# Kernel optimization log

Measured on AMD Instinct MI355X. Metric: run time of the kernel, lower is better.

## Reference

```python
import jax, jax.numpy as jnp
import numpy as np

D = 4  # max horizontal displacement


def setup_inputs() -> dict:
    key = jax.random.key(0)
    k1, k2 = jax.random.split(key)
    feat1 = jax.random.normal(k1, (8, 256, 96, 320), dtype=jnp.float32)
    feat2 = jax.random.normal(k2, (8, 256, 96, 320), dtype=jnp.float32)
    return {"feat1": feat1, "feat2": feat2}


def reference(feat1, feat2):
    B, C, H, W = feat1.shape
    # zero-pad feat2 along width by D on each side
    feat2_padded = jnp.pad(feat2, ((0, 0), (0, 0), (0, 0), (D, D)))
    costs = []
    for i in range(2 * D + 1):  # small fixed loop over 2d+1 shifts
        feat2_slice = jax.lax.dynamic_slice_in_dim(feat2_padded, i, W, axis=3)
        # channel-mean correlation -> (B, H, W)
        costs.append(jnp.mean(feat1 * feat2_slice, axis=1))
    # stack shifts as channels -> (B, 2d+1, H, W)
    return jnp.stack(costs, axis=1)
```

## Files before the change

### kernel.cpp

```cpp
#include <hip/hip_runtime.h>


constexpr int B  = 8;
constexpr int C  = 256;
constexpr int H  = 96;
constexpr int W  = 320;
constexpr int NS = 9;
constexpr int QT = W / 4;
constexpr int RPB = 3;
constexpr int NTH = RPB * QT;
constexpr int HW  = H * W;
constexpr int PADW = W + 8;
constexpr int NSTEP = C / 2;

__global__ __launch_bounds__(NTH, 1)
void cv_kernel(const float* __restrict__ f1,
               const float* __restrict__ f2,
               float* __restrict__ out) {
    __shared__ float buf[4][RPB][PADW];

    const int tid = threadIdx.x;
    const int q   = tid % QT;
    const int r   = tid / QT;

    const int blk = blockIdx.x;
    const int hb  = blk % (H / RPB);
    const int b   = blk / (H / RPB);
    const int h   = hb * RPB + r;

    const float* p1 = f1 + ((size_t)b * C * H + (size_t)h) * W + 4 * q;
    const float* p2 = f2 + ((size_t)b * C * H + (size_t)h) * W + 4 * q;

    if (q == 0) {
#pragma unroll
        for (int p = 0; p < 4; ++p)
#pragma unroll
            for (int k = 0; k < 4; ++k) buf[p][r][k] = 0.f;
    }
    if (q == QT - 1) {
#pragma unroll
        for (int p = 0; p < 4; ++p)
#pragma unroll
            for (int k = 0; k < 4; ++k) buf[p][r][4 + W + k] = 0.f;
    }

    float acc[4][NS];
#pragma unroll
    for (int j = 0; j < 4; ++j)
#pragma unroll
        for (int s = 0; s < NS; ++s) acc[j][s] = 0.0f;

    float4 a0 = *reinterpret_cast<const float4*>(p1);
    float4 r0 = *reinterpret_cast<const float4*>(p2);
    float4 a1 = *reinterpret_cast<const float4*>(p1 + (size_t)HW);
    float4 r1 = *reinterpret_cast<const float4*>(p2 + (size_t)HW);
    float4 a2 = *reinterpret_cast<const float4*>(p1 + 2 * (size_t)HW);
    float4 r2 = *reinterpret_cast<const float4*>(p2 + 2 * (size_t)HW);
    float4 a3 = *reinterpret_cast<const float4*>(p1 + 3 * (size_t)HW);
    float4 r3 = *reinterpret_cast<const float4*>(p2 + 3 * (size_t)HW);
    float4 a4 = *reinterpret_cast<const float4*>(p1 + 4 * (size_t)HW);
    float4 r4 = *reinterpret_cast<const float4*>(p2 + 4 * (size_t)HW);
    float4 a5 = *reinterpret_cast<const float4*>(p1 + 5 * (size_t)HW);
    float4 r5 = *reinterpret_cast<const float4*>(p2 + 5 * (size_t)HW);
    int cL = 6;

#define CV_FMA(AV, X0, RM, X2)                                             \
    {                                                                      \
        const float xw[12] = {X0.x, X0.y, X0.z, X0.w,                      \
                              RM.x, RM.y, RM.z, RM.w,                      \
                              X2.x, X2.y, X2.z, X2.w};                     \
        const float av[4] = {AV.x, AV.y, AV.z, AV.w};                      \
        _Pragma("unroll")                                                  \
        for (int j = 0; j < 4; ++j)                                        \
            _Pragma("unroll")                                              \
            for (int s = 0; s < NS; ++s)                                   \
                acc[j][s] = fmaf(av[j], xw[j + s], acc[j][s]);             \
    }

#define STEP(P0, P1)                                                       \
    {                                                                      \
        *reinterpret_cast<float4*>(&buf[P0][r][4 + 4 * q]) = r0;           \
        *reinterpret_cast<float4*>(&buf[P1][r][4 + 4 * q]) = r1;           \
        const float4 aL0 = *reinterpret_cast<const float4*>(               \
            p1 + (size_t)cL * HW);                                         \
        const float4 rL0 = *reinterpret_cast<const float4*>(               \
            p2 + (size_t)cL * HW);                                         \
        const float4 aL1 = *reinterpret_cast<const float4*>(               \
            p1 + (size_t)(cL + 1) * HW);                                   \
        const float4 rL1 = *reinterpret_cast<const float4*>(               \
            p2 + (size_t)(cL + 1) * HW);                                   \
        cL = (cL < C - 2) ? cL + 2 : cL;                                   \
        asm volatile("s_waitcnt lgkmcnt(0)" ::: "memory");                 \
        __builtin_amdgcn_s_barrier();                                      \
        asm volatile("" ::: "memory");                                     \
        const float4 x0a =                                                 \
            *reinterpret_cast<const float4*>(&buf[P0][r][4 * q]);          \
        const float4 x2a =                                                 \
            *reinterpret_cast<const float4*>(&buf[P0][r][4 * q + 8]);      \
        const float4 x0b =                                                 \
            *reinterpret_cast<const float4*>(&buf[P1][r][4 * q]);          \
        const float4 x2b =                                                 \
            *reinterpret_cast<const float4*>(&buf[P1][r][4 * q + 8]);      \
        CV_FMA(a0, x0a, r0, x2a)                                           \
        CV_FMA(a1, x0b, r1, x2b)                                           \
        a0 = a2; r0 = r2; a1 = a3; r1 = r3;                                \
        a2 = a4; r2 = r4; a3 = a5; r3 = r5;                                \
        a4 = aL0; r4 = rL0; a5 = aL1; r5 = rL1;                            \
    }

#pragma unroll 1
    for (int s = 0; s < NSTEP; s += 2) {
        STEP(0, 1)
        STEP(2, 3)
    }
#undef STEP
#undef CV_FMA

    const float scale = 1.0f / (float)C;
    float* obase = out + (((size_t)b * NS) * H + h) * (size_t)W + 4 * q;
#pragma unroll
    for (int s = 0; s < NS; ++s) {
        float4 v = make_float4(acc[0][s] * scale, acc[1][s] * scale,
                               acc[2][s] * scale, acc[3][s] * scale);
        *reinterpret_cast<float4*>(obase + (size_t)s * HW) = v;
    }
}

extern "C" void kernel_launch(void* const* d_in, const int* in_sizes, int n_in,
                              void* d_out, int out_size, void* d_ws, size_t ws_size,
                              hipStream_t stream) {
    const float* f1 = (const float*)d_in[0];
    const float* f2 = (const float*)d_in[1];
    float* out = (float*)d_out;

    dim3 grid(B * (H / RPB));
    dim3 block(NTH);
    hipLaunchKernelGGL(cv_kernel, grid, block, 0, stream, f1, f2, out);
}
```

Before: 92.78 us.

## Split channel reduction across two thread groups per block with LDS combine

```diff
diff --git a/kernel.cpp b/kernel.cpp
--- a/kernel.cpp
+++ b/kernel.cpp
@@ -8,40 +8,47 @@
 constexpr int NS = 9;
 constexpr int QT = W / 4;
 constexpr int RPB = 3;
-constexpr int NTH = RPB * QT;
+constexpr int CG  = 2;
+constexpr int TPG = RPB * QT;
+constexpr int NTH = CG * TPG;
+constexpr int CPG = C / CG;
 constexpr int HW  = H * W;
 constexpr int PADW = W + 8;
-constexpr int NSTEP = C / 2;
+constexpr int NSTEP = CPG / 2;
 
 __global__ __launch_bounds__(NTH, 1)
 void cv_kernel(const float* __restrict__ f1,
                const float* __restrict__ f2,
                float* __restrict__ out) {
-    __shared__ float buf[4][RPB][PADW];
+    __shared__ float buf[4][CG][RPB][PADW];
 
     const int tid = threadIdx.x;
-    const int q   = tid % QT;
-    const int r   = tid / QT;
+    const int cg  = tid / TPG;
+    const int t   = tid % TPG;
+    const int q   = t % QT;
+    const int r   = t / QT;
 
     const int blk = blockIdx.x;
     const int hb  = blk % (H / RPB);
     const int b   = blk / (H / RPB);
     const int h   = hb * RPB + r;
 
-    const float* p1 = f1 + ((size_t)b * C * H + (size_t)h) * W + 4 * q;
-    const float* p2 = f2 + ((size_t)b * C * H + (size_t)h) * W + 4 * q;
+    const float* p1 =
+        f1 + (((size_t)b * C + (size_t)cg * CPG) * H + (size_t)h) * W + 4 * q;
+    const float* p2 =
+        f2 + (((size_t)b * C + (size_t)cg * CPG) * H + (size_t)h) * W + 4 * q;
 
     if (q == 0) {
 #pragma unroll
         for (int p = 0; p < 4; ++p)
 #pragma unroll
-            for (int k = 0; k < 4; ++k) buf[p][r][k] = 0.f;
+            for (int k = 0; k < 4; ++k) buf[p][cg][r][k] = 0.f;
     }
     if (q == QT - 1) {
 #pragma unroll
         for (int p = 0; p < 4; ++p)
 #pragma unroll
-            for (int k = 0; k < 4; ++k) buf[p][r][4 + W + k] = 0.f;
+            for (int k = 0; k < 4; ++k) buf[p][cg][r][4 + W + k] = 0.f;
     }
 
     float acc[4][NS];
@@ -79,8 +86,8 @@
 
 #define STEP(P0, P1)                                                       \
     {                                                                      \
-        *reinterpret_cast<float4*>(&buf[P0][r][4 + 4 * q]) = r0;           \
-        *reinterpret_cast<float4*>(&buf[P1][r][4 + 4 * q]) = r1;           \
+        *reinterpret_cast<float4*>(&buf[P0][cg][r][4 + 4 * q]) = r0;       \
+        *reinterpret_cast<float4*>(&buf[P1][cg][r][4 + 4 * q]) = r1;       \
         const float4 aL0 = *reinterpret_cast<const float4*>(               \
             p1 + (size_t)cL * HW);                                         \
         const float4 rL0 = *reinterpret_cast<const float4*>(               \
@@ -89,18 +96,18 @@
             p1 + (size_t)(cL + 1) * HW);                                   \
         const float4 rL1 = *reinterpret_cast<const float4*>(               \
             p2 + (size_t)(cL + 1) * HW);                                   \
-        cL = (cL < C - 2) ? cL + 2 : cL;                                   \
+        cL = (cL < CPG - 2) ? cL + 2 : cL;                                 \
         asm volatile("s_waitcnt lgkmcnt(0)" ::: "memory");                 \
         __builtin_amdgcn_s_barrier();                                      \
         asm volatile("" ::: "memory");                                     \
         const float4 x0a =                                                 \
-            *reinterpret_cast<const float4*>(&buf[P0][r][4 * q]);          \
+            *reinterpret_cast<const float4*>(&buf[P0][cg][r][4 * q]);      \
         const float4 x2a =                                                 \
-            *reinterpret_cast<const float4*>(&buf[P0][r][4 * q + 8]);      \
+            *reinterpret_cast<const float4*>(&buf[P0][cg][r][4 * q + 8]);  \
         const float4 x0b =                                                 \
-            *reinterpret_cast<const float4*>(&buf[P1][r][4 * q]);          \
+            *reinterpret_cast<const float4*>(&buf[P1][cg][r][4 * q]);      \
         const float4 x2b =                                                 \
-            *reinterpret_cast<const float4*>(&buf[P1][r][4 * q + 8]);      \
+            *reinterpret_cast<const float4*>(&buf[P1][cg][r][4 * q + 8]);  \
         CV_FMA(a0, x0a, r0, x2a)                                           \
         CV_FMA(a1, x0b, r1, x2b)                                           \
         a0 = a2; r0 = r2; a1 = a3; r1 = r3;                                \
@@ -117,12 +124,24 @@
 #undef CV_FMA
 
     const float scale = 1.0f / (float)C;
+    float* stage = &buf[0][0][0][0];
     float* obase = out + (((size_t)b * NS) * H + h) * (size_t)W + 4 * q;
-#pragma unroll
+#pragma unroll 1
     for (int s = 0; s < NS; ++s) {
-        float4 v = make_float4(acc[0][s] * scale, acc[1][s] * scale,
-                               acc[2][s] * scale, acc[3][s] * scale);
-        *reinterpret_cast<float4*>(obase + (size_t)s * HW) = v;
+        __syncthreads();
+        if (cg == 1) {
+            *reinterpret_cast<float4*>(&stage[4 * t]) =
+                make_float4(acc[0][s], acc[1][s], acc[2][s], acc[3][s]);
+        }
+        __syncthreads();
+        if (cg == 0) {
+            const float4 o = *reinterpret_cast<const float4*>(&stage[4 * t]);
+            float4 v = make_float4((acc[0][s] + o.x) * scale,
+                                   (acc[1][s] + o.y) * scale,
+                                   (acc[2][s] + o.z) * scale,
+                                   (acc[3][s] + o.w) * scale);
+            *reinterpret_cast<float4*>(obase + (size_t)s * HW) = v;
+        }
     }
 }
 
```

Measured after the change: 112.9 us, median of 2. 21.7% more time.
